# Kernel tuning notes

Measured on AMD Instinct MI355X. Metric: run time of the kernel, lower is better.

Reference implementation:

```python
import jax, jax.numpy as jnp
import numpy as np

B_SZ, SEQ, D_MODEL = 2, 512, 1024
EXPAND, HEAD_DIM = 2, 64
D_INNER = EXPAND * D_MODEL            # 2048
N_HEADS = D_INNER // HEAD_DIM         # 32
D_STATE = 64
EPS = 1e-6
PROJ_DIM = 2 * D_INNER + 2 * N_HEADS * D_STATE + N_HEADS  # 8224


def setup_inputs() -> dict:
    key = jax.random.key(0)
    k = jax.random.split(key, 5)
    return {
        "hidden": jax.random.normal(k[0], (B_SZ, SEQ, D_MODEL), jnp.float32),
        "W_in": 0.02 * jax.random.normal(k[1], (D_MODEL, PROJ_DIM), jnp.float32),
        "dt_bias": 0.5 * jax.random.normal(k[2], (N_HEADS,), jnp.float32),
        "A_log": 0.5 * jax.random.normal(k[3], (N_HEADS,), jnp.float32),
        "norm_weight": jnp.ones((D_INNER,), jnp.float32),
        "W_out": 0.02 * jax.random.normal(k[4], (D_INNER, D_MODEL), jnp.float32),
    }


def _rope(x, theta):
    # x: [b,l,h,n] interleaved pairs (view_as_complex convention); theta: [b,l,h,n//2]
    x0, x1 = x[..., 0::2], x[..., 1::2]
    c, s = jnp.cos(theta), jnp.sin(theta)
    y = jnp.stack([x0 * c - x1 * s, x0 * s + x1 * c], axis=-1)
    return y.reshape(x.shape)


def reference(hidden, W_in, dt_bias, A_log, norm_weight, W_out):
    b, l, _ = hidden.shape
    proj = hidden @ W_in  # [b,l,PROJ_DIM]
    hn = N_HEADS * D_STATE
    z = proj[..., :D_INNER]
    xr = proj[..., D_INNER:2 * D_INNER].reshape(b, l, N_HEADS, HEAD_DIM)
    Bm = proj[..., 2 * D_INNER:2 * D_INNER + hn].reshape(b, l, N_HEADS, D_STATE)
    Cm = proj[..., 2 * D_INNER + hn:2 * D_INNER + 2 * hn].reshape(b, l, N_HEADS, D_STATE)
    dt = jax.nn.softplus(proj[..., -N_HEADS:] + dt_bias)  # [b,l,h]

    A = -jnp.exp(A_log)                 # [h], negative decay
    alpha = jnp.exp(dt * A)             # decay factor
    beta = 0.5 * dt * alpha             # trapezoidal: half-step on previous input
    gamma = 0.5 * dt                    # trapezoidal: half-step on current input

    # data-dependent RoPE: phase is cumulative dt scaled by per-dim inverse freq
    half = D_STATE // 2
    inv_freq = 1.0 / (10000.0 ** (jnp.arange(half, dtype=jnp.float32) / half))
    theta = jnp.cumsum(dt, axis=1)[..., None] * inv_freq  # [b,l,h,half]
    Bm = _rope(Bm, theta)
    Cm = _rope(Cm, theta)

    # shifted (t-1) inputs, zero at t=0 (h starts at 0 so alpha-at-t0 is a no-op)
    Bp = jnp.pad(Bm[:, :-1], ((0, 0), (1, 0), (0, 0), (0, 0)))
    xp = jnp.pad(xr[:, :-1], ((0, 0), (1, 0), (0, 0), (0, 0)))

    tl = lambda t: jnp.moveaxis(t, 1, 0)  # time-major for scan
    xs = (tl(xr), tl(Bm), tl(Cm), tl(Bp), tl(xp), tl(alpha), tl(beta), tl(gamma))
    h0 = jnp.zeros((b, N_HEADS, D_STATE, HEAD_DIM), hidden.dtype)

    def step(h, inp):
        x_t, B_t, C_t, Bprev, xprev, a, bt, g = inp
        h = (a[..., None, None] * h
             + bt[..., None, None] * jnp.einsum('bhn,bhp->bhnp', Bprev, xprev)
             + g[..., None, None] * jnp.einsum('bhn,bhp->bhnp', B_t, x_t))
        y = jnp.einsum('bhn,bhnp->bhp', C_t, h)
        return h, y

    _, ys = jax.lax.scan(step, h0, xs)          # ys: [l,b,h,p]
    y = jnp.moveaxis(ys, 0, 1).reshape(b, l, D_INNER)

    y = y * jax.nn.silu(z)                      # gated output
    rms = jnp.sqrt(jnp.mean(y * y, axis=-1, keepdims=True) + EPS)
    y = y / rms * norm_weight                   # RMSNorm
    return y @ W_out
```

## Files before the change

kernel.cpp:

```cpp
#include <hip/hip_runtime.h>
#include <stdint.h>

typedef __attribute__((ext_vector_type(8))) short short8;
typedef __attribute__((ext_vector_type(8))) unsigned short ushort8;
typedef __attribute__((ext_vector_type(4))) unsigned short usv4;
typedef __attribute__((ext_vector_type(4))) float float4v;

#define B_SZ 2
#define SEQ 512
#define D_MODEL 1024
#define D_INNER 2048
#define N_HEADS 32
#define HEAD_DIM 64
#define D_STATE 64
#define PROJ_DIM 8224
#define NPAD 8320
#define MROWS 1024

__device__ __forceinline__ unsigned short f2bf(float f) {
    unsigned u = __builtin_bit_cast(unsigned, f);
    u += 0x7fffu + ((u >> 16) & 1u);
    return (unsigned short)(u >> 16);
}
__device__ __forceinline__ float bf2f(unsigned short h) {
    return __builtin_bit_cast(float, (unsigned)h << 16);
}

__device__ __forceinline__ void gld16(unsigned short* lds, const unsigned short* g) {
#if __has_builtin(__builtin_amdgcn_global_load_lds)
    __builtin_amdgcn_global_load_lds(
        (const __attribute__((address_space(1))) void*)g,
        (__attribute__((address_space(3))) void*)lds, 16, 0, 0);
#else
    *(short8*)lds = *(const short8*)g;
#endif
}

__device__ void transpose_body(const float* __restrict__ src,
                               unsigned short* __restrict__ dst,
                               int R, int C, int bx, int by, float* T, int tid) {
    int c0 = bx * 64, r0 = by * 64;
    int row = tid >> 2, cg = (tid & 3) * 16;
    #pragma unroll
    for (int k = 0; k < 4; k++) {
        int col = cg + k * 4;
        float4v v;
        if (c0 + col + 3 < C) {
            v = *(const float4v*)&src[(size_t)(r0 + row) * C + c0 + col];
        } else {
            #pragma unroll
            for (int e = 0; e < 4; e++)
                v[e] = (c0 + col + e < C) ? src[(size_t)(r0 + row) * C + c0 + col + e] : 0.f;
        }
        *(float4v*)&T[row * 68 + col] = v;
    }
    __syncthreads();
    int drow = tid >> 2, sg = (tid & 3) * 16;
    ushort8 v[2];
    #pragma unroll
    for (int k = 0; k < 16; k++) v[k >> 3][k & 7] = f2bf(T[(sg + k) * 68 + drow]);
    unsigned short* d = &dst[(size_t)(c0 + drow) * R + r0 + sg];
    *(ushort8*)&d[0] = v[0];
    *(ushort8*)&d[8] = v[1];
}

__global__ __launch_bounds__(256) void prep_fat(
    const float* __restrict__ hidden, const float* __restrict__ W_in,
    const float* __restrict__ W_out, unsigned short* __restrict__ Hb,
    unsigned short* __restrict__ Wt1, unsigned short* __restrict__ Wt2) {
    __shared__ float T[64 * 68];
    int blk = blockIdx.x, tid = threadIdx.x;
    if (blk < 1024) {
        int i = blk * 1024 + tid * 4;
        float4v v = *(const float4v*)&hidden[i];
        usv4 o;
        #pragma unroll
        for (int k = 0; k < 4; k++) o[k] = f2bf(v[k]);
        *(usv4*)&Hb[i] = o;
    } else if (blk < 3104) {
        int q = blk - 1024;
        transpose_body(W_in, Wt1, D_MODEL, PROJ_DIM, q % 130, q / 130, T, tid);
    } else {
        int q = blk - 3104;
        transpose_body(W_out, Wt2, D_INNER, D_MODEL, q % 16, q / 16, T, tid);
    }
}

template <bool BF16OUT>
__global__ __launch_bounds__(256) void gemm_bt(
    const unsigned short* __restrict__ A, const unsigned short* __restrict__ Bt,
    void* __restrict__ Cout, int M, int N, int K, int klen) {
    __shared__ unsigned short As[8192];
    __shared__ unsigned short Bs[8192];
    int tid = threadIdx.x;
    int lane = tid & 63, w = tid >> 6, quad = lane >> 4, l15 = lane & 15;
    int m0 = blockIdx.y * 128, n0 = blockIdx.x * 128;
    int kb = blockIdx.z * klen, ke = kb + klen;
    int wm = (w & 1) * 64, wn = (w >> 1) * 64;
    float4v acc[4][4];
    #pragma unroll
    for (int i = 0; i < 4; i++)
        #pragma unroll
        for (int j = 0; j < 4; j++) acc[i][j] = (float4v){0.f, 0.f, 0.f, 0.f};

    int rs = tid >> 3;
    int gl = ((tid & 7) ^ (rs & 7)) * 8;
    const unsigned short* ap = &A [(size_t)(m0 + rs) * K + gl];
    const unsigned short* bp = &Bt[(size_t)(n0 + rs) * K + gl];
    int rx = l15 & 7;

    for (int k0 = kb; k0 < ke; k0 += 64) {
        __syncthreads();
        #pragma unroll
        for (int p = 0; p < 4; p++) {
            gld16(&As[p * 2048 + tid * 8], ap + (size_t)(p * 32) * K + k0);
            gld16(&Bs[p * 2048 + tid * 8], bp + (size_t)(p * 32) * K + k0);
        }
        __syncthreads();
        #pragma unroll
        for (int kq = 0; kq < 2; kq++) {
            short8 af[4], bfr[4];
            #pragma unroll
            for (int mt = 0; mt < 4; mt++)
                af[mt] = *(const short8*)&As[(wm + mt * 16 + l15) * 64 + (((kq << 2) + quad) ^ rx) * 8];
            #pragma unroll
            for (int nt = 0; nt < 4; nt++)
                bfr[nt] = *(const short8*)&Bs[(wn + nt * 16 + l15) * 64 + (((kq << 2) + quad) ^ rx) * 8];
            #pragma unroll
            for (int mt = 0; mt < 4; mt++)
                #pragma unroll
                for (int nt = 0; nt < 4; nt++)
                    acc[mt][nt] = __builtin_amdgcn_mfma_f32_16x16x32_bf16(
                        af[mt], bfr[nt], acc[mt][nt], 0, 0, 0);
        }
    }
    #pragma unroll
    for (int mt = 0; mt < 4; mt++)
        #pragma unroll
        for (int nt = 0; nt < 4; nt++)
            #pragma unroll
            for (int r = 0; r < 4; r++) {
                int row = m0 + wm + mt * 16 + quad * 4 + r;
                int col = n0 + wn + nt * 16 + l15;
                if (col < N) {
                    if (BF16OUT)
                        ((unsigned short*)Cout)[(size_t)blockIdx.z * M * N + (size_t)row * N + col]
                            = f2bf(acc[mt][nt][r]);
                    else
                        ((float*)Cout)[(size_t)blockIdx.z * M * N + (size_t)row * N + col]
                            = acc[mt][nt][r];
                }
            }
}

__global__ __launch_bounds__(256) void reduce4(
    const float* __restrict__ P, float* __restrict__ out, int n) {
    int i = (blockIdx.x * 256 + threadIdx.x) * 4;
    float4v s = *(const float4v*)&P[i];
    #pragma unroll
    for (int z = 1; z < 4; z++) {
        float4v v = *(const float4v*)&P[(size_t)z * n + i];
        #pragma unroll
        for (int k = 0; k < 4; k++) s[k] += v[k];
    }
    *(float4v*)&out[i] = s;
}

__global__ __launch_bounds__(256) void headprep(
    const unsigned short* __restrict__ proj, const float* __restrict__ dt_bias,
    float* __restrict__ dt_arr, float* __restrict__ cum_arr,
    unsigned short* __restrict__ Bh, unsigned short* __restrict__ Ch,
    unsigned short* __restrict__ Xt) {
    __shared__ float dtS[SEQ];
    __shared__ float cumS[SEQ];
    __shared__ unsigned short XT[128 * 72];
    int bh = blockIdx.x;
    int b = bh >> 5, h = bh & 31;
    int tid = threadIdx.x, lane = tid & 63, w = tid >> 6;

    if (w == 0) {
        float bias = dt_bias[h];
        float carry = 0.f;
        for (int c = 0; c < 8; c++) {
            int t = c * 64 + lane;
            float raw = bf2f(proj[(size_t)(b * SEQ + t) * PROJ_DIM + 8192 + h]) + bias;
            float dt = raw > 20.f ? raw : log1pf(expf(raw));
            float v = dt;
            #pragma unroll
            for (int d = 1; d < 64; d <<= 1) {
                float nv = __shfl_up(v, d, 64);
                if (lane >= d) v += nv;
            }
            float cum = carry + v;
            dtS[t] = dt; cumS[t] = cum;
            dt_arr[bh * SEQ + t] = dt;
            cum_arr[bh * SEQ + t] = cum;
            carry = __shfl(cum, 63, 64);
        }
    }
    __syncthreads();

    int j = tid & 31, t8 = tid >> 5;
    const float k_l2 = 13.287712379549449f / 32.f;
    float freq = exp2f(-(float)j * k_l2);
    for (int pass = 0; pass < 64; pass++) {
        int t = pass * 8 + t8;
        float th = cumS[t] * freq;
        float s, c;
        __sincosf(th, &s, &c);
        size_t rb = (size_t)(b * SEQ + t) * PROJ_DIM;
        unsigned bu = *(const unsigned*)&proj[rb + 4096 + h * 64 + 2 * j];
        unsigned cu = *(const unsigned*)&proj[rb + 6144 + h * 64 + 2 * j];
        float b0 = bf2f((unsigned short)(bu & 0xffff)), b1 = bf2f((unsigned short)(bu >> 16));
        float c0 = bf2f((unsigned short)(cu & 0xffff)), c1 = bf2f((unsigned short)(cu >> 16));
        size_t dst = ((size_t)bh * SEQ + t) * 64 + 2 * j;
        unsigned ob = (unsigned)f2bf(b0 * c - b1 * s) | ((unsigned)f2bf(b0 * s + b1 * c) << 16);
        unsigned oc = (unsigned)f2bf(c0 * c - c1 * s) | ((unsigned)f2bf(c0 * s + c1 * c) << 16);
        *(unsigned*)&Bh[dst] = ob;
        *(unsigned*)&Ch[dst] = oc;
    }

    for (int ch = 0; ch < 4; ch++) {
        __syncthreads();
        #pragma unroll
        for (int r = 0; r < 4; r++) {
            int idx = r * 2048 + tid * 8;
            int tl = idx >> 6, pp = idx & 63;
            *(ushort8*)&XT[tl * 72 + pp] =
                *(const ushort8*)&proj[(size_t)(b * SEQ + ch * 128 + tl) * PROJ_DIM + 2048 + h * 64 + pp];
        }
        __syncthreads();
        int p = tid & 63, sq = tid >> 6;
        #pragma unroll
        for (int r = 0; r < 4; r++) {
            int s0 = r * 32 + sq * 8;
            ushort8 v;
            #pragma unroll
            for (int k = 0; k < 8; k++) v[k] = XT[(s0 + k) * 72 + p];
            *(ushort8*)&Xt[((size_t)bh * 64 + p) * SEQ + ch * 128 + s0] = v;
        }
    }
}

__global__ __launch_bounds__(256) void attn_scan(
    const unsigned short* __restrict__ Bh, const unsigned short* __restrict__ Ch,
    const unsigned short* __restrict__ Xt, const float* __restrict__ dt_arr,
    const float* __restrict__ cum_arr, const float* __restrict__ A_log,
    float* __restrict__ y_ws) {
    __shared__ unsigned short Bs[4096];
    __shared__ unsigned short Xs[4096];
    __shared__ unsigned short Ps[4096];
    int qt = blockIdx.x, bh = blockIdx.y;
    int b = bh >> 5, h = bh & 31;
    float Aneg = -expf(A_log[h]);
    int tid = threadIdx.x, lane = tid & 63, w = tid >> 6;
    int quad = lane >> 4, l15 = lane & 15;

    int qrow = qt * 64 + w * 16 + l15;
    const unsigned short* Cptr = Ch + ((size_t)bh * SEQ + qrow) * 64;
    short8 cf[2];
    cf[0] = *(const short8*)&Cptr[quad * 8];
    cf[1] = *(const short8*)&Cptr[32 + quad * 8];

    int trow[4];
    float cumt[4];
    #pragma unroll
    for (int r = 0; r < 4; r++) {
        trow[r] = qt * 64 + w * 16 + quad * 4 + r;
        cumt[r] = cum_arr[bh * SEQ + trow[r]];
    }
    float4v yacc[4];
    #pragma unroll
    for (int i = 0; i < 4; i++) yacc[i] = (float4v){0.f, 0.f, 0.f, 0.f};

    for (int st = 0; st <= qt; st++) {
        __syncthreads();
        const unsigned short* bsrc = Bh + ((size_t)bh * SEQ + st * 64) * 64;
        gld16(&Bs[tid * 8],         bsrc + tid * 8);
        gld16(&Bs[(tid + 256) * 8], bsrc + (tid + 256) * 8);
        const unsigned short* xsrc = Xt + (size_t)bh * 64 * SEQ + st * 64;
        {
            int e = tid;
            int p = e >> 3, so = (e & 7) * 8;
            gld16(&Xs[p * 64 + so], xsrc + (size_t)p * SEQ + so);
            e = tid + 256;
            p = e >> 3; so = (e & 7) * 8;
            gld16(&Xs[p * 64 + so], xsrc + (size_t)p * SEQ + so);
        }
        __syncthreads();
        float4v sacc[4];
        #pragma unroll
        for (int i = 0; i < 4; i++) sacc[i] = (float4v){0.f, 0.f, 0.f, 0.f};
        #pragma unroll
        for (int kk = 0; kk < 2; kk++)
            #pragma unroll
            for (int nt = 0; nt < 4; nt++) {
                short8 bf8 = *(const short8*)&Bs[(nt * 16 + l15) * 64 + kk * 32 + quad * 8];
                sacc[nt] = __builtin_amdgcn_mfma_f32_16x16x32_bf16(cf[kk], bf8, sacc[nt], 0, 0, 0);
            }
        #pragma unroll
        for (int nt = 0; nt < 4; nt++) {
            int s = st * 64 + nt * 16 + l15;
            float cums = cum_arr[bh * SEQ + s];
            float dts = dt_arr[bh * SEQ + s];
            float dts1 = (s + 1 < SEQ) ? dt_arr[bh * SEQ + s + 1] : 0.f;
            #pragma unroll
            for (int r = 0; r < 4; r++) {
                int t = trow[r];
                float wgt = (s > t) ? 0.f
                          : expf(Aneg * (cumt[r] - cums)) * 0.5f * (dts + ((s < t) ? dts1 : 0.f));
                Ps[w * 1024 + (quad * 4 + r) * 64 + nt * 16 + l15] = f2bf(sacc[nt][r] * wgt);
            }
        }
        __syncthreads();
        #pragma unroll
        for (int kk = 0; kk < 2; kk++) {
            short8 af = *(const short8*)&Ps[w * 1024 + l15 * 64 + kk * 32 + quad * 8];
            #pragma unroll
            for (int pt = 0; pt < 4; pt++) {
                short8 xf = *(const short8*)&Xs[(pt * 16 + l15) * 64 + kk * 32 + quad * 8];
                yacc[pt] = __builtin_amdgcn_mfma_f32_16x16x32_bf16(af, xf, yacc[pt], 0, 0, 0);
            }
        }
    }
    #pragma unroll
    for (int pt = 0; pt < 4; pt++)
        #pragma unroll
        for (int r = 0; r < 4; r++) {
            int t = trow[r];
            int p = pt * 16 + l15;
            y_ws[((size_t)b * SEQ + t) * D_INNER + h * 64 + p] = yacc[pt][r];
        }
}

__global__ __launch_bounds__(256) void gated_rmsnorm(
    const float* __restrict__ y_ws, const unsigned short* __restrict__ proj,
    const float* __restrict__ nw, unsigned short* __restrict__ Y2) {
    __shared__ float red[4];
    int m = blockIdx.x, tid = threadIdx.x;
    const float* yrow = y_ws + (size_t)m * D_INNER;
    const unsigned short* zrow = proj + (size_t)m * PROJ_DIM;
    int j0 = tid * 8;
    ushort8 zv = *(const ushort8*)&zrow[j0];
    float v[8];
    float ss = 0.f;
    #pragma unroll
    for (int k = 0; k < 8; k++) {
        float y = yrow[j0 + k];
        float z = bf2f(zv[k]);
        float g = y * (z / (1.f + expf(-z)));
        v[k] = g;
        ss += g * g;
    }
    #pragma unroll
    for (int d = 32; d > 0; d >>= 1) ss += __shfl_down(ss, d, 64);
    if ((tid & 63) == 0) red[tid >> 6] = ss;
    __syncthreads();
    float tot = red[0] + red[1] + red[2] + red[3];
    float inv = 1.0f / sqrtf(tot / (float)D_INNER + 1e-6f);
    #pragma unroll
    for (int k = 0; k < 8; k++)
        Y2[(size_t)m * D_INNER + j0 + k] = f2bf(v[k] * inv * nw[j0 + k]);
}


extern "C" void kernel_launch(void* const* d_in, const int* in_sizes, int n_in,
                              void* d_out, int out_size, void* d_ws, size_t ws_size,
                              hipStream_t stream) {
    const float* hidden   = (const float*)d_in[0];
    const float* W_in     = (const float*)d_in[1];
    const float* dt_bias  = (const float*)d_in[2];
    const float* A_log    = (const float*)d_in[3];
    const float* norm_w   = (const float*)d_in[4];
    const float* W_out    = (const float*)d_in[5];
    float* out = (float*)d_out;

    char* ws = (char*)d_ws;
    unsigned short* Wt1  = (unsigned short*)(ws);
    unsigned short* Hb   = (unsigned short*)(ws + 17039360);
    unsigned short* proj = (unsigned short*)(ws + 19136512);
    float* dt_arr        = (float*)(ws + 35979264);
    float* cum_arr       = (float*)(ws + 36110336);
    unsigned short* Bh   = (unsigned short*)(ws + 36241408);
    unsigned short* Ch   = (unsigned short*)(ws + 40435712);
    unsigned short* Xt   = (unsigned short*)(ws + 44630016);
    float* y_ws          = (float*)(ws + 48824320);
    unsigned short* Y2   = (unsigned short*)(ws + 57212928);
    unsigned short* Wt2  = (unsigned short*)(ws + 61407232);
    float* Pk = (float*)proj;

    prep_fat<<<3616, 256, 0, stream>>>(hidden, W_in, W_out, Hb, Wt1, Wt2);
    gemm_bt<true><<<dim3(NPAD / 128, MROWS / 128, 1), 256, 0, stream>>>(
        Hb, Wt1, proj, MROWS, PROJ_DIM, D_MODEL, D_MODEL);
    headprep<<<64, 256, 0, stream>>>(proj, dt_bias, dt_arr, cum_arr, Bh, Ch, Xt);
    attn_scan<<<dim3(8, 64), 256, 0, stream>>>(Bh, Ch, Xt, dt_arr, cum_arr, A_log, y_ws);
    gated_rmsnorm<<<MROWS, 256, 0, stream>>>(y_ws, proj, norm_w, Y2);
    gemm_bt<false><<<dim3(D_MODEL / 128, MROWS / 128, 4), 256, 0, stream>>>(
        Y2, Wt2, Pk, MROWS, D_MODEL, D_INNER, D_INNER / 4);
    reduce4<<<MROWS * D_MODEL / 1024, 256, 0, stream>>>(Pk, out, MROWS * D_MODEL);
}
```

Baseline: 211.0 us.

## Split headprep into parallel dt scan and wide RoPE/transpose packing kernel

The single 64-block headprep kernel is replaced by two kernels. A dt_scan kernel computes softplus and the cumulative sum with all four waves and a shared-memory carry. A 1536-block pack_fat kernel then applies RoPE per token row and transposes X in 64x64 tiles. This spreads the memory-bound packing work across far more blocks than 64 to fill the GPU, at the cost of an extra launch and a round trip of cum_arr through global memory.

```diff
diff --git a/kernel.cpp b/kernel.cpp
--- a/kernel.cpp
+++ b/kernel.cpp
@@ -166,79 +166,83 @@
     *(float4v*)&out[i] = s;
 }
 
-__global__ __launch_bounds__(256) void headprep(
+__global__ __launch_bounds__(256) void dt_scan(
     const unsigned short* __restrict__ proj, const float* __restrict__ dt_bias,
-    float* __restrict__ dt_arr, float* __restrict__ cum_arr,
-    unsigned short* __restrict__ Bh, unsigned short* __restrict__ Ch,
-    unsigned short* __restrict__ Xt) {
-    __shared__ float dtS[SEQ];
-    __shared__ float cumS[SEQ];
-    __shared__ unsigned short XT[128 * 72];
+    float* __restrict__ dt_arr, float* __restrict__ cum_arr) {
+    __shared__ float chs[8];
     int bh = blockIdx.x;
     int b = bh >> 5, h = bh & 31;
     int tid = threadIdx.x, lane = tid & 63, w = tid >> 6;
-
-    if (w == 0) {
-        float bias = dt_bias[h];
-        float carry = 0.f;
-        for (int c = 0; c < 8; c++) {
-            int t = c * 64 + lane;
-            float raw = bf2f(proj[(size_t)(b * SEQ + t) * PROJ_DIM + 8192 + h]) + bias;
-            float dt = raw > 20.f ? raw : log1pf(expf(raw));
-            float v = dt;
-            #pragma unroll
-            for (int d = 1; d < 64; d <<= 1) {
-                float nv = __shfl_up(v, d, 64);
-                if (lane >= d) v += nv;
-            }
-            float cum = carry + v;
-            dtS[t] = dt; cumS[t] = cum;
-            dt_arr[bh * SEQ + t] = dt;
-            cum_arr[bh * SEQ + t] = cum;
-            carry = __shfl(cum, 63, 64);
-        }
-    }
+    float bias = dt_bias[h];
+    int t0 = w * 64 + lane, t1 = 256 + w * 64 + lane;
+    float raw0 = bf2f(proj[(size_t)(b * SEQ + t0) * PROJ_DIM + 8192 + h]) + bias;
+    float raw1 = bf2f(proj[(size_t)(b * SEQ + t1) * PROJ_DIM + 8192 + h]) + bias;
+    float dt0 = raw0 > 20.f ? raw0 : log1pf(expf(raw0));
+    float dt1 = raw1 > 20.f ? raw1 : log1pf(expf(raw1));
+    float v0 = dt0, v1 = dt1;
+    #pragma unroll
+    for (int d = 1; d < 64; d <<= 1) {
+        float n0 = __shfl_up(v0, d, 64);
+        float n1 = __shfl_up(v1, d, 64);
+        if (lane >= d) { v0 += n0; v1 += n1; }
+    }
+    if (lane == 63) { chs[w] = v0; chs[4 + w] = v1; }
     __syncthreads();
-
-    int j = tid & 31, t8 = tid >> 5;
-    const float k_l2 = 13.287712379549449f / 32.f;
-    float freq = exp2f(-(float)j * k_l2);
-    for (int pass = 0; pass < 64; pass++) {
-        int t = pass * 8 + t8;
-        float th = cumS[t] * freq;
-        float s, c;
-        __sincosf(th, &s, &c);
-        size_t rb = (size_t)(b * SEQ + t) * PROJ_DIM;
-        unsigned bu = *(const unsigned*)&proj[rb + 4096 + h * 64 + 2 * j];
-        unsigned cu = *(const unsigned*)&proj[rb + 6144 + h * 64 + 2 * j];
-        float b0 = bf2f((unsigned short)(bu & 0xffff)), b1 = bf2f((unsigned short)(bu >> 16));
-        float c0 = bf2f((unsigned short)(cu & 0xffff)), c1 = bf2f((unsigned short)(cu >> 16));
-        size_t dst = ((size_t)bh * SEQ + t) * 64 + 2 * j;
-        unsigned ob = (unsigned)f2bf(b0 * c - b1 * s) | ((unsigned)f2bf(b0 * s + b1 * c) << 16);
-        unsigned oc = (unsigned)f2bf(c0 * c - c1 * s) | ((unsigned)f2bf(c0 * s + c1 * c) << 16);
-        *(unsigned*)&Bh[dst] = ob;
-        *(unsigned*)&Ch[dst] = oc;
-    }
-
-    for (int ch = 0; ch < 4; ch++) {
-        __syncthreads();
-        #pragma unroll
-        for (int r = 0; r < 4; r++) {
-            int idx = r * 2048 + tid * 8;
-            int tl = idx >> 6, pp = idx & 63;
-            *(ushort8*)&XT[tl * 72 + pp] =
-                *(const ushort8*)&proj[(size_t)(b * SEQ + ch * 128 + tl) * PROJ_DIM + 2048 + h * 64 + pp];
-        }
-        __syncthreads();
-        int p = tid & 63, sq = tid >> 6;
-        #pragma unroll
-        for (int r = 0; r < 4; r++) {
-            int s0 = r * 32 + sq * 8;
-            ushort8 v;
-            #pragma unroll
-            for (int k = 0; k < 8; k++) v[k] = XT[(s0 + k) * 72 + p];
-            *(ushort8*)&Xt[((size_t)bh * 64 + p) * SEQ + ch * 128 + s0] = v;
-        }
+    float off0 = 0.f, off1 = 0.f;
+    #pragma unroll
+    for (int c = 0; c < 8; c++) {
+        float s = chs[c];
+        if (c < w) off0 += s;
+        if (c < 4 + w) off1 += s;
+    }
+    dt_arr[bh * SEQ + t0] = dt0;  cum_arr[bh * SEQ + t0] = off0 + v0;
+    dt_arr[bh * SEQ + t1] = dt1;  cum_arr[bh * SEQ + t1] = off1 + v1;
+}
+
+__global__ __launch_bounds__(256) void pack_fat(
+    const unsigned short* __restrict__ proj, const float* __restrict__ cum_arr,
+    unsigned short* __restrict__ Bh, unsigned short* __restrict__ Ch,
+    unsigned short* __restrict__ Xt) {
+    __shared__ unsigned short XT[64 * 72];
+    int blk = blockIdx.x, tid = threadIdx.x;
+    if (blk < 1024) {
+        int m = blk, b = m >> 9, t = m & 511;
+        const float k_l2 = 13.287712379549449f / 32.f;
+        #pragma unroll
+        for (int i = 0; i < 4; i++) {
+            int q = i * 256 + tid;
+            int h = q >> 5, j = q & 31;
+            float cum = cum_arr[(b * 32 + h) * SEQ + t];
+            float th = cum * exp2f(-(float)j * k_l2);
+            float s, c;
+            __sincosf(th, &s, &c);
+            size_t rb = (size_t)m * PROJ_DIM;
+            unsigned bu = *(const unsigned*)&proj[rb + 4096 + h * 64 + 2 * j];
+            unsigned cu = *(const unsigned*)&proj[rb + 6144 + h * 64 + 2 * j];
+            float b0 = bf2f((unsigned short)(bu & 0xffff)), b1 = bf2f((unsigned short)(bu >> 16));
+            float c0 = bf2f((unsigned short)(cu & 0xffff)), c1 = bf2f((unsigned short)(cu >> 16));
+            size_t dst = ((size_t)(b * 32 + h) * SEQ + t) * 64 + 2 * j;
+            unsigned ob = (unsigned)f2bf(b0 * c - b1 * s) | ((unsigned)f2bf(b0 * s + b1 * c) << 16);
+            unsigned oc = (unsigned)f2bf(c0 * c - c1 * s) | ((unsigned)f2bf(c0 * s + c1 * c) << 16);
+            *(unsigned*)&Bh[dst] = ob;
+            *(unsigned*)&Ch[dst] = oc;
+        }
+    } else {
+        int q = blk - 1024;
+        int bh = q >> 3, s0 = (q & 7) * 64;
+        int b = bh >> 5, h = bh & 31;
+        int r = tid >> 2, cg = (tid & 3) * 16;
+        const unsigned short* src = &proj[(size_t)(b * SEQ + s0 + r) * PROJ_DIM + 2048 + h * 64 + cg];
+        *(ushort8*)&XT[r * 72 + cg]     = *(const ushort8*)&src[0];
+        *(ushort8*)&XT[r * 72 + cg + 8] = *(const ushort8*)&src[8];
+        __syncthreads();
+        int p = tid >> 2, sg = (tid & 3) * 16;
+        ushort8 v[2];
+        #pragma unroll
+        for (int k = 0; k < 16; k++) v[k >> 3][k & 7] = XT[(sg + k) * 72 + p];
+        unsigned short* dst = &Xt[((size_t)bh * 64 + p) * SEQ + s0 + sg];
+        *(ushort8*)&dst[0] = v[0];
+        *(ushort8*)&dst[8] = v[1];
     }
 }
 
@@ -392,7 +396,8 @@
     prep_fat<<<3616, 256, 0, stream>>>(hidden, W_in, W_out, Hb, Wt1, Wt2);
     gemm_bt<true><<<dim3(NPAD / 128, MROWS / 128, 1), 256, 0, stream>>>(
         Hb, Wt1, proj, MROWS, PROJ_DIM, D_MODEL, D_MODEL);
-    headprep<<<64, 256, 0, stream>>>(proj, dt_bias, dt_arr, cum_arr, Bh, Ch, Xt);
+    dt_scan<<<64, 256, 0, stream>>>(proj, dt_bias, dt_arr, cum_arr);
+    pack_fat<<<1536, 256, 0, stream>>>(proj, cum_arr, Bh, Ch, Xt);
     attn_scan<<<dim3(8, 64), 256, 0, stream>>>(Bh, Ch, Xt, dt_arr, cum_arr, A_log, y_ws);
     gated_rmsnorm<<<MROWS, 256, 0, stream>>>(y_ws, proj, norm_w, Y2);
     gemm_bt<false><<<dim3(D_MODEL / 128, MROWS / 128, 4), 256, 0, stream>>>(
```

Result: faster. 194.5 us (-7.8%).
